# Kernel tuning notes

Hardware: AMD Instinct MI355X
Metric: run time of the kernel (lower is better)

The kernel has to match this reference:

```python
import jax, jax.numpy as jnp
import numpy as np


def setup_inputs() -> dict:
    key = jax.random.key(0)
    k1, k2 = jax.random.split(key)
    img_render_points = jax.random.normal(k1, (128, 128, 2), dtype=jnp.float32)
    ref_catheter_contour_point_cloud = jax.random.normal(k2, (16384, 2), dtype=jnp.float32)
    return {
        "img_render_points": img_render_points,
        "ref_catheter_contour_point_cloud": ref_catheter_contour_point_cloud,
    }


def reference(img_render_points, ref_catheter_contour_point_cloud):
    # Flatten to point cloud (N, 2)
    pc = img_render_points.reshape(-1, 2)
    ref = ref_catheter_contour_point_cloud  # (M, 2)
    # Pairwise Euclidean distances (N, M); torch.norm(..., dim=2) equivalent
    diff = pc[:, None, :] - ref[None, :, :]          # (N, M, 2)
    distances = jnp.sqrt(jnp.sum(diff * diff, axis=-1))  # (N, M)
    min_d1 = jnp.min(distances, axis=1)  # nearest ref point for each render point
    min_d2 = jnp.min(distances, axis=0)  # nearest render point for each ref point
    chamfer_loss = jnp.sum(min_d1) + jnp.sum(min_d2)
    return chamfer_loss
```

## Files before the change

kernel.cpp:

```cpp
#include <hip/hip_runtime.h>
#include <math.h>


#define NPTS  16384
#define BLK   256
#define TCH   16
#define CHUNK (NPTS / TCH)
#define TT    (CHUNK / 16)
#define QPB   512
#define QBN   (NPTS / QPB)
#define SCALE 16.0f
#define INVS  0.0625f

typedef _Float16 f16x8 __attribute__((ext_vector_type(8)));
typedef float    f32x4 __attribute__((ext_vector_type(4)));


__global__ __launch_bounds__(BLK, 4) void cc_min_kernel(
        const float2* __restrict__ pc,
        const float2* __restrict__ ref,
        float* __restrict__ ws,
        float* __restrict__ out) {
    __shared__ f16x8 sB[CHUNK];

    const int b    = blockIdx.x;
    const int dir  = b / (QBN * TCH);
    const int rem  = b % (QBN * TCH);
    const int qblk = rem / TCH;
    const int ch   = rem % TCH;
    const int tid  = threadIdx.x;
    const int wid  = tid >> 6;
    const int lane = tid & 63;

    if (b == 0 && tid == 0) out[0] = 0.0f;

    const float2* __restrict__ qry = dir ? ref : pc;
    const float2* __restrict__ tgt = dir ? pc  : ref;

#pragma unroll
    for (int r = 0; r < CHUNK / BLK; ++r) {
        int i = r * BLK + tid;
        float2 t = tgt[ch * CHUNK + i];
        float xs = t.x * SCALE, ys = t.y * SCALE;
        _Float16 hx = (_Float16)xs; _Float16 lx = (_Float16)(xs - (float)hx);
        _Float16 hy = (_Float16)ys; _Float16 ly = (_Float16)(ys - (float)hy);
        float zz = fmaf(xs, xs, ys * ys);
        _Float16 hz = (_Float16)zz; _Float16 lz = (_Float16)(zz - (float)hz);
        f16x8 p;
        p[0] = (_Float16)(-2.0f * (float)hx);
        p[1] = (_Float16)(-2.0f * (float)lx);
        p[2] = p[0];
        p[3] = (_Float16)(-2.0f * (float)hy);
        p[4] = (_Float16)(-2.0f * (float)ly);
        p[5] = p[3];
        p[6] = hz;
        p[7] = lz;
        sB[i] = p;
    }

    const int q0 = qblk * QPB + wid * 128;
    f16x8 A[8];
#pragma unroll
    for (int qt = 0; qt < 8; ++qt) {
        f16x8 a;
#pragma unroll
        for (int e = 0; e < 8; ++e) a[e] = (_Float16)0.0f;
        if (lane < 16) {
            float2 qp = qry[q0 + qt * 16 + lane];
            float xs = qp.x * SCALE, ys = qp.y * SCALE;
            _Float16 hx = (_Float16)xs; _Float16 lx = (_Float16)(xs - (float)hx);
            _Float16 hy = (_Float16)ys; _Float16 ly = (_Float16)(ys - (float)hy);
            a[0] = hx; a[1] = hx; a[2] = lx;
            a[3] = hy; a[4] = hy; a[5] = ly;
            a[6] = (_Float16)1.0f; a[7] = (_Float16)1.0f;
        }
        A[qt] = a;
    }
    __syncthreads();

    f32x4 m[8];
#pragma unroll
    for (int qt = 0; qt < 8; ++qt)
        m[qt] = (f32x4){INFINITY, INFINITY, INFINITY, INFINITY};

    const f32x4 Z4 = (f32x4){0.f, 0.f, 0.f, 0.f};
    const int bo = lane & 15;
    for (int tt = 0; tt < TT; tt += 2) {
        f16x8 b0 = sB[tt * 16 + bo];
        f16x8 b1 = sB[tt * 16 + 16 + bo];
#pragma unroll
        for (int qt = 0; qt < 8; ++qt) {
            f32x4 d0 = __builtin_amdgcn_mfma_f32_16x16x32_f16(A[qt], b0, Z4, 0, 0, 0);
            f32x4 d1 = __builtin_amdgcn_mfma_f32_16x16x32_f16(A[qt], b1, Z4, 0, 0, 0);
#pragma unroll
            for (int r = 0; r < 4; ++r)
                m[qt][r] = fminf(fminf(m[qt][r], d0[r]), d1[r]);
        }
    }

#pragma unroll
    for (int qt = 0; qt < 8; ++qt) {
#pragma unroll
        for (int r = 0; r < 4; ++r) {
            float v = m[qt][r];
            v = fminf(v, __shfl_xor(v, 1, 16));
            v = fminf(v, __shfl_xor(v, 2, 16));
            v = fminf(v, __shfl_xor(v, 4, 16));
            v = fminf(v, __shfl_xor(v, 8, 16));
            m[qt][r] = v;
        }
    }

    if ((lane & 15) == 0) {
        int rowbase = (lane >> 4) * 4;
        float* prow = ws + (size_t)ch * (2 * NPTS) + dir * NPTS;
#pragma unroll
        for (int qt = 0; qt < 8; ++qt) {
            float4 v = make_float4(m[qt][0], m[qt][1], m[qt][2], m[qt][3]);
            *(float4*)(prow + q0 + qt * 16 + rowbase) = v;
        }
    }
}

__global__ __launch_bounds__(BLK) void cc_final_kernel(
        const float2* __restrict__ pc, const float2* __restrict__ ref,
        const float* __restrict__ ws, float* __restrict__ out) {
    int q = blockIdx.x * BLK + threadIdx.x;

    float m0 = INFINITY, m1 = INFINITY, m2 = INFINITY, m3 = INFINITY;
#pragma unroll
    for (int ch = 0; ch < TCH; ch += 4) {
        m0 = fminf(m0, ws[(size_t)(ch + 0) * (2 * NPTS) + q]);
        m1 = fminf(m1, ws[(size_t)(ch + 1) * (2 * NPTS) + q]);
        m2 = fminf(m2, ws[(size_t)(ch + 2) * (2 * NPTS) + q]);
        m3 = fminf(m3, ws[(size_t)(ch + 3) * (2 * NPTS) + q]);
    }
    float msur = fminf(fminf(m0, m1), fminf(m2, m3));

    int dir = q >> 14, qi = q & (NPTS - 1);
    float2 p = dir ? ref[qi] : pc[qi];
    float pn = (SCALE * SCALE) * fmaf(p.x, p.x, p.y * p.y);
    float s = sqrtf(fmaxf(msur + pn, 0.0f)) * INVS;

#pragma unroll
    for (int off = 32; off > 0; off >>= 1)
        s += __shfl_down(s, off, 64);

    if ((threadIdx.x & 63) == 0)
        atomicAdd(out, s);
}

extern "C" void kernel_launch(void* const* d_in, const int* in_sizes, int n_in,
                              void* d_out, int out_size, void* d_ws, size_t ws_size,
                              hipStream_t stream) {
    const float2* pc  = (const float2*)d_in[0];
    const float2* ref = (const float2*)d_in[1];
    float* out = (float*)d_out;
    float* ws  = (float*)d_ws;

    cc_min_kernel<<<2 * QBN * TCH, BLK, 0, stream>>>(pc, ref, ws, out);
    cc_final_kernel<<<(2 * NPTS) / BLK, BLK, 0, stream>>>(pc, ref, ws, out);
}
```

Baseline: 87.24 us.

## Prepack target table and stream full target set per query block via async LDS loads

Adds a pack kernel that converts targets once into the f16 split-precision MFMA operand table. The min kernel drops the per-block target chunking: each block covers 64 queries against all 16384 targets, streamed through double-buffered LDS with global_load_lds, and the two wave halves are merged in shared memory. The final reduction kernel and the partial-min workspace round trip go away because sqrt and sum are done in-kernel with one atomic per block. The trade is that each wave now holds one A tile, so it gets less register reuse per B load than the previous eight, and the grid is 512 blocks, which may limit latency hiding.

```diff
diff --git a/kernel.cpp b/kernel.cpp
--- a/kernel.cpp
+++ b/kernel.cpp
@@ -3,12 +3,10 @@
 
 
 #define NPTS  16384
-#define BLK   256
-#define TCH   16
-#define CHUNK (NPTS / TCH)
-#define TT    (CHUNK / 16)
-#define QPB   512
-#define QBN   (NPTS / QPB)
+#define BLK   512
+#define QPB   64
+#define NCH   16
+#define CH    1024
 #define SCALE 16.0f
 #define INVS  0.0625f
 
@@ -16,138 +14,142 @@
 typedef float    f32x4 __attribute__((ext_vector_type(4)));
 
 
+__device__ __forceinline__ void gload16(const void* g, void* l) {
+    __builtin_amdgcn_global_load_lds(
+        (const __attribute__((address_space(1))) unsigned int*)g,
+        (__attribute__((address_space(3))) unsigned int*)l, 16, 0, 0);
+}
+
+__global__ __launch_bounds__(256) void cc_pack_kernel(
+        const float2* __restrict__ pc, const float2* __restrict__ ref,
+        f16x8* __restrict__ tbl, float* __restrict__ out) {
+    int idx = blockIdx.x * 256 + threadIdx.x;
+    if (idx == 0) out[0] = 0.0f;
+    int dir = idx >> 14;
+    int i   = idx & (NPTS - 1);
+    float2 t = dir ? pc[i] : ref[i];
+    float xs = t.x * SCALE, ys = t.y * SCALE;
+    _Float16 hx = (_Float16)xs; _Float16 lx = (_Float16)(xs - (float)hx);
+    _Float16 hy = (_Float16)ys; _Float16 ly = (_Float16)(ys - (float)hy);
+    float zz = fmaf(xs, xs, ys * ys);
+    _Float16 hz = (_Float16)zz; _Float16 lz = (_Float16)(zz - (float)hz);
+    f16x8 p;
+    p[0] = (_Float16)(-2.0f * (float)hx);
+    p[1] = (_Float16)(-2.0f * (float)lx);
+    p[2] = p[0];
+    p[3] = (_Float16)(-2.0f * (float)hy);
+    p[4] = (_Float16)(-2.0f * (float)ly);
+    p[5] = p[3];
+    p[6] = hz;
+    p[7] = lz;
+    tbl[idx] = p;
+}
+
 __global__ __launch_bounds__(BLK, 4) void cc_min_kernel(
-        const float2* __restrict__ pc,
-        const float2* __restrict__ ref,
-        float* __restrict__ ws,
-        float* __restrict__ out) {
-    __shared__ f16x8 sB[CHUNK];
+        const float2* __restrict__ pc, const float2* __restrict__ ref,
+        const f16x8* __restrict__ tbl, float* __restrict__ out) {
+    __shared__ f16x8 stage[2][2 * CH];
+    __shared__ f32x4 xbuf[4][64];
+    __shared__ float psum[16];
 
     const int b    = blockIdx.x;
-    const int dir  = b / (QBN * TCH);
-    const int rem  = b % (QBN * TCH);
-    const int qblk = rem / TCH;
-    const int ch   = rem % TCH;
+    const int dir  = b >> 8;
+    const int qblk = b & 255;
     const int tid  = threadIdx.x;
-    const int wid  = tid >> 6;
+    const int w    = tid >> 6;
     const int lane = tid & 63;
-
-    if (b == 0 && tid == 0) out[0] = 0.0f;
+    const int half = w >> 2;
+    const int qt   = w & 3;
 
     const float2* __restrict__ qry = dir ? ref : pc;
-    const float2* __restrict__ tgt = dir ? pc  : ref;
+    const f16x8*  __restrict__ tb  = tbl + dir * NPTS;
+
+    const int q0 = qblk * QPB + qt * 16;
+    f16x8 A;
+#pragma unroll
+    for (int e = 0; e < 8; ++e) A[e] = (_Float16)0.0f;
+    if (lane < 16) {
+        float2 qp = qry[q0 + lane];
+        float xs = qp.x * SCALE, ys = qp.y * SCALE;
+        _Float16 hx = (_Float16)xs; _Float16 lx = (_Float16)(xs - (float)hx);
+        _Float16 hy = (_Float16)ys; _Float16 ly = (_Float16)(ys - (float)hy);
+        A[0] = hx; A[1] = hx; A[2] = lx;
+        A[3] = hy; A[4] = hy; A[5] = ly;
+        A[6] = (_Float16)1.0f; A[7] = (_Float16)1.0f;
+    }
+
+    const int lo = w * 1024;
+#define STAGE(buf, c)                                                        \
+    {                                                                        \
+        const char* g0 = (const char*)(tb + (c) * CH);                       \
+        const char* g1 = (const char*)(tb + (8 + (c)) * CH);                 \
+        char* lb = (char*)&stage[buf][0];                                    \
+        gload16(g0 + lo + lane * 16,          lb + lo);                      \
+        gload16(g0 + lo + 8192 + lane * 16,   lb + lo + 8192);               \
+        gload16(g1 + lo + lane * 16,          lb + lo + 16384);              \
+        gload16(g1 + lo + 8192 + lane * 16,   lb + lo + 24576);              \
+    }
+
+    f32x4 m = (f32x4){INFINITY, INFINITY, INFINITY, INFINITY};
+    const f32x4 Z4 = (f32x4){0.f, 0.f, 0.f, 0.f};
+    const int bo = lane & 15;
+
+    STAGE(0, 0);
+    __syncthreads();
+
+    for (int c = 0; c < 8; ++c) {
+        if (c < 7) STAGE((c + 1) & 1, c + 1);
+        const f16x8* S = &stage[c & 1][half * CH];
+#pragma unroll 8
+        for (int tt = 0; tt < 64; tt += 2) {
+            f16x8 b0 = S[tt * 16 + bo];
+            f16x8 b1 = S[tt * 16 + 16 + bo];
+            f32x4 d0 = __builtin_amdgcn_mfma_f32_16x16x32_f16(A, b0, Z4, 0, 0, 0);
+            f32x4 d1 = __builtin_amdgcn_mfma_f32_16x16x32_f16(A, b1, Z4, 0, 0, 0);
+#pragma unroll
+            for (int r = 0; r < 4; ++r)
+                m[r] = fminf(fminf(m[r], d0[r]), d1[r]);
+        }
+        __syncthreads();
+    }
+
+    if (half) *(f32x4*)&xbuf[qt][lane] = m;
+    __syncthreads();
+    if (!half) {
+        f32x4 o = *(const f32x4*)&xbuf[qt][lane];
+#pragma unroll
+        for (int r = 0; r < 4; ++r) m[r] = fminf(m[r], o[r]);
 
 #pragma unroll
-    for (int r = 0; r < CHUNK / BLK; ++r) {
-        int i = r * BLK + tid;
-        float2 t = tgt[ch * CHUNK + i];
-        float xs = t.x * SCALE, ys = t.y * SCALE;
-        _Float16 hx = (_Float16)xs; _Float16 lx = (_Float16)(xs - (float)hx);
-        _Float16 hy = (_Float16)ys; _Float16 ly = (_Float16)(ys - (float)hy);
-        float zz = fmaf(xs, xs, ys * ys);
-        _Float16 hz = (_Float16)zz; _Float16 lz = (_Float16)(zz - (float)hz);
-        f16x8 p;
-        p[0] = (_Float16)(-2.0f * (float)hx);
-        p[1] = (_Float16)(-2.0f * (float)lx);
-        p[2] = p[0];
-        p[3] = (_Float16)(-2.0f * (float)hy);
-        p[4] = (_Float16)(-2.0f * (float)ly);
-        p[5] = p[3];
-        p[6] = hz;
-        p[7] = lz;
-        sB[i] = p;
-    }
-
-    const int q0 = qblk * QPB + wid * 128;
-    f16x8 A[8];
-#pragma unroll
-    for (int qt = 0; qt < 8; ++qt) {
-        f16x8 a;
-#pragma unroll
-        for (int e = 0; e < 8; ++e) a[e] = (_Float16)0.0f;
-        if (lane < 16) {
-            float2 qp = qry[q0 + qt * 16 + lane];
-            float xs = qp.x * SCALE, ys = qp.y * SCALE;
-            _Float16 hx = (_Float16)xs; _Float16 lx = (_Float16)(xs - (float)hx);
-            _Float16 hy = (_Float16)ys; _Float16 ly = (_Float16)(ys - (float)hy);
-            a[0] = hx; a[1] = hx; a[2] = lx;
-            a[3] = hy; a[4] = hy; a[5] = ly;
-            a[6] = (_Float16)1.0f; a[7] = (_Float16)1.0f;
-        }
-        A[qt] = a;
-    }
-    __syncthreads();
-
-    f32x4 m[8];
-#pragma unroll
-    for (int qt = 0; qt < 8; ++qt)
-        m[qt] = (f32x4){INFINITY, INFINITY, INFINITY, INFINITY};
-
-    const f32x4 Z4 = (f32x4){0.f, 0.f, 0.f, 0.f};
-    const int bo = lane & 15;
-    for (int tt = 0; tt < TT; tt += 2) {
-        f16x8 b0 = sB[tt * 16 + bo];
-        f16x8 b1 = sB[tt * 16 + 16 + bo];
-#pragma unroll
-        for (int qt = 0; qt < 8; ++qt) {
-            f32x4 d0 = __builtin_amdgcn_mfma_f32_16x16x32_f16(A[qt], b0, Z4, 0, 0, 0);
-            f32x4 d1 = __builtin_amdgcn_mfma_f32_16x16x32_f16(A[qt], b1, Z4, 0, 0, 0);
-#pragma unroll
-            for (int r = 0; r < 4; ++r)
-                m[qt][r] = fminf(fminf(m[qt][r], d0[r]), d1[r]);
-        }
-    }
-
-#pragma unroll
-    for (int qt = 0; qt < 8; ++qt) {
-#pragma unroll
         for (int r = 0; r < 4; ++r) {
-            float v = m[qt][r];
+            float v = m[r];
             v = fminf(v, __shfl_xor(v, 1, 16));
             v = fminf(v, __shfl_xor(v, 2, 16));
             v = fminf(v, __shfl_xor(v, 4, 16));
             v = fminf(v, __shfl_xor(v, 8, 16));
-            m[qt][r] = v;
+            m[r] = v;
+        }
+
+        if ((lane & 15) == 0) {
+            int g = lane >> 4;
+            float ssum = 0.0f;
+#pragma unroll
+            for (int r = 0; r < 4; ++r) {
+                float2 qp = qry[q0 + g * 4 + r];
+                float xs = qp.x * SCALE, ys = qp.y * SCALE;
+                float pn = fmaf(xs, xs, ys * ys);
+                ssum += sqrtf(fmaxf(m[r] + pn, 0.0f));
+            }
+            psum[w * 4 + g] = ssum;
         }
     }
-
-    if ((lane & 15) == 0) {
-        int rowbase = (lane >> 4) * 4;
-        float* prow = ws + (size_t)ch * (2 * NPTS) + dir * NPTS;
+    __syncthreads();
+    if (tid == 0) {
+        float t = 0.0f;
 #pragma unroll
-        for (int qt = 0; qt < 8; ++qt) {
-            float4 v = make_float4(m[qt][0], m[qt][1], m[qt][2], m[qt][3]);
-            *(float4*)(prow + q0 + qt * 16 + rowbase) = v;
-        }
+        for (int k = 0; k < 16; ++k) t += psum[k];
+        atomicAdd(out, t * INVS);
     }
-}
-
-__global__ __launch_bounds__(BLK) void cc_final_kernel(
-        const float2* __restrict__ pc, const float2* __restrict__ ref,
-        const float* __restrict__ ws, float* __restrict__ out) {
-    int q = blockIdx.x * BLK + threadIdx.x;
-
-    float m0 = INFINITY, m1 = INFINITY, m2 = INFINITY, m3 = INFINITY;
-#pragma unroll
-    for (int ch = 0; ch < TCH; ch += 4) {
-        m0 = fminf(m0, ws[(size_t)(ch + 0) * (2 * NPTS) + q]);
-        m1 = fminf(m1, ws[(size_t)(ch + 1) * (2 * NPTS) + q]);
-        m2 = fminf(m2, ws[(size_t)(ch + 2) * (2 * NPTS) + q]);
-        m3 = fminf(m3, ws[(size_t)(ch + 3) * (2 * NPTS) + q]);
-    }
-    float msur = fminf(fminf(m0, m1), fminf(m2, m3));
-
-    int dir = q >> 14, qi = q & (NPTS - 1);
-    float2 p = dir ? ref[qi] : pc[qi];
-    float pn = (SCALE * SCALE) * fmaf(p.x, p.x, p.y * p.y);
-    float s = sqrtf(fmaxf(msur + pn, 0.0f)) * INVS;
-
-#pragma unroll
-    for (int off = 32; off > 0; off >>= 1)
-        s += __shfl_down(s, off, 64);
-
-    if ((threadIdx.x & 63) == 0)
-        atomicAdd(out, s);
 }
 
 extern "C" void kernel_launch(void* const* d_in, const int* in_sizes, int n_in,
@@ -156,8 +158,8 @@
     const float2* pc  = (const float2*)d_in[0];
     const float2* ref = (const float2*)d_in[1];
     float* out = (float*)d_out;
-    float* ws  = (float*)d_ws;
+    f16x8* tbl = (f16x8*)d_ws;
 
-    cc_min_kernel<<<2 * QBN * TCH, BLK, 0, stream>>>(pc, ref, ws, out);
-    cc_final_kernel<<<(2 * NPTS) / BLK, BLK, 0, stream>>>(pc, ref, ws, out);
+    cc_pack_kernel<<<(2 * NPTS) / 256, 256, 0, stream>>>(pc, ref, tbl, out);
+    cc_min_kernel<<<512, BLK, 0, stream>>>(pc, ref, tbl, out);
 }
```

After: 85.08 us. 2.5% less time.
